# Kernel tuning notes

Measured on AMD Instinct MI355X. Metric: run time of the kernel, lower is better.

The kernel has to match this reference:

```python
import jax, jax.numpy as jnp
import numpy as np


def setup_inputs() -> dict:
    key = jax.random.key(0)
    ks = jax.random.split(key, 9)
    N, L, E, H = 8, 4096, 1024, 16
    D = E // H
    return {
        "values": jax.random.normal(ks[0], (N, L, E), dtype=jnp.float32),
        "keys": jax.random.normal(ks[1], (N, L, E), dtype=jnp.float32),
        "query": jax.random.normal(ks[2], (N, L, E), dtype=jnp.float32),
        "mask": jax.random.randint(ks[3], (1, 1, H, H), 0, 2, dtype=jnp.int32),
        "Wv": jax.random.normal(ks[4], (D, D), dtype=jnp.float32) / np.sqrt(D),
        "Wk": jax.random.normal(ks[5], (D, D), dtype=jnp.float32) / np.sqrt(D),
        "Wq": jax.random.normal(ks[6], (D, D), dtype=jnp.float32) / np.sqrt(D),
        "Wo": jax.random.normal(ks[7], (E, E), dtype=jnp.float32) / np.sqrt(E),
        "bo": jnp.zeros((E,), dtype=jnp.float32),
    }


def reference(values, keys, query, mask, Wv, Wk, Wq, Wo, bo):
    N, L, E = query.shape
    H = mask.shape[-1]          # heads
    D = E // H                  # head_dim
    # reshape to (N, L, H, D) then per-head Dense(head_dim) on last dim
    v = values.reshape(N, L, H, D) @ Wv
    k = keys.reshape(N, L, H, D) @ Wk
    q = query.reshape(N, L, H, D) @ Wq
    # Faithful to the source: keys transposed with perm [0,1,3,2], so matmul
    # batches over (N, L) and energy is a (H x H) matrix per position.
    energy = jnp.einsum("nlhd,nlgd->nlhg", q, k)  # (N, L, H, H)
    energy = jnp.where(mask == 0, jnp.float32(-1e20), energy)
    attention = jax.nn.softmax(energy / (E ** 0.5), axis=-1)
    out = jnp.einsum("nlhg,nlgd->nlhd", attention, v)  # (N, L, H, D)
    # source: transpose to (N, H, L, D) then reshape to (N, L, H*D)
    out = out.transpose(0, 2, 1, 3).reshape(N, L, H * D)
    out = out @ Wo + bo
    return out, attention
```

## Files before the change

kernel.cpp:

```cpp
#include <hip/hip_runtime.h>

typedef short short8 __attribute__((ext_vector_type(8)));
typedef float f32x4 __attribute__((ext_vector_type(4)));
typedef unsigned short u16;

#define MFMA16(a, b, c) __builtin_amdgcn_mfma_f32_16x16x32_bf16(a, b, c, 0, 0, 0)
#define GLD_LDS(g, l)                                                          \
  __builtin_amdgcn_global_load_lds(                                            \
      (__attribute__((address_space(1))) void*)(void*)(g),                     \
      (__attribute__((address_space(3))) void*)(l), 16, 0, 0)

__device__ __forceinline__ u16 f2bf(float f) {
  union { float f; unsigned u; } x; x.f = f;
  unsigned r = x.u + 0x7fffu + ((x.u >> 16) & 1u);
  return (u16)(r >> 16);
}

__device__ __forceinline__ short8 pack8(float4 a, float4 b) {
  short8 r;
  r[0] = (short)f2bf(a.x); r[1] = (short)f2bf(a.y);
  r[2] = (short)f2bf(a.z); r[3] = (short)f2bf(a.w);
  r[4] = (short)f2bf(b.x); r[5] = (short)f2bf(b.y);
  r[6] = (short)f2bf(b.z); r[7] = (short)f2bf(b.w);
  return r;
}

__global__ __launch_bounds__(256) void prep(const float* __restrict__ Wv,
                                            const float* __restrict__ Wk,
                                            const float* __restrict__ Wq,
                                            const float* __restrict__ Wo,
                                            u16* __restrict__ WoT2,
                                            u16* __restrict__ Mt) {
  __shared__ __align__(16) float A[64][65];
  __shared__ __align__(16) float B[64][68];
  const int t = threadIdx.x;
  const int r = t >> 2, c = (t & 3) * 16;
  if (blockIdx.x < 256) {
    const int tr = blockIdx.x >> 4, tc = blockIdx.x & 15;
#pragma unroll
    for (int u = 0; u < 4; ++u)
      *(float4*)&A[r][c + u * 4] = *(const float4*)(Wv + r * 64 + c + u * 4);
#pragma unroll
    for (int u = 0; u < 4; ++u)
      *(float4*)&B[r][c + u * 4] =
          *(const float4*)(Wo + (tr * 64 + r) * 1024 + tc * 64 + c + u * 4);
    __syncthreads();
    const int n = t & 63, i0 = (t >> 6) * 16;
    float acc[16];
#pragma unroll
    for (int ii = 0; ii < 16; ++ii) acc[ii] = 0.f;
    for (int j = 0; j < 64; ++j) {
      const float wo = B[j][n];
#pragma unroll
      for (int ii = 0; ii < 16; ++ii) acc[ii] += A[i0 + ii][j] * wo;
    }
    u16* dst = WoT2 + (size_t)(tc * 64 + n) * 1024 + tr * 64 + i0;
    short8 o0, o1;
#pragma unroll
    for (int jj = 0; jj < 8; ++jj) { o0[jj] = (short)f2bf(acc[jj]); o1[jj] = (short)f2bf(acc[8 + jj]); }
    *(short8*)(void*)dst = o0;
    *(short8*)(void*)(dst + 8) = o1;
  } else {
#pragma unroll
    for (int u = 0; u < 4; ++u)
      *(float4*)&A[r][c + u * 4] = *(const float4*)(Wq + r * 64 + c + u * 4);
#pragma unroll
    for (int u = 0; u < 4; ++u)
      *(float4*)&B[r][c + u * 4] = *(const float4*)(Wk + r * 64 + c + u * 4);
    __syncthreads();
    const int n = t & 63, k0 = (t >> 6) * 16;
    float acc[16];
#pragma unroll
    for (int ii = 0; ii < 16; ++ii) acc[ii] = 0.f;
    for (int d = 0; d < 64; ++d) {
      const float wk = B[n][d];
#pragma unroll
      for (int kk = 0; kk < 16; ++kk) acc[kk] += A[k0 + kk][d] * wk;
    }
    u16* dst = Mt + n * 64 + k0;
    short8 o0, o1;
#pragma unroll
    for (int jj = 0; jj < 8; ++jj) { o0[jj] = (short)f2bf(acc[jj]); o1[jj] = (short)f2bf(acc[8 + jj]); }
    *(short8*)(void*)dst = o0;
    *(short8*)(void*)(dst + 8) = o1;
  }
}

__global__ __launch_bounds__(256, 3) void attn_kernel(
    const float* __restrict__ values, const float* __restrict__ keys,
    const float* __restrict__ query, const int* __restrict__ mask,
    const u16* __restrict__ Mt, float* __restrict__ attn,
    u16* __restrict__ out2) {
  __shared__ __align__(16) u16 t_lds[4][16][72];
  __shared__ __align__(16) u16 vT_lds[4][64][24];
  __shared__ __align__(16) u16 p_lds[4][16][24];

  const int tid = threadIdx.x;
  const int w = tid >> 6, lane = tid & 63;
  const int g16 = lane & 15;
  const int q4 = lane >> 4;
  const int kbase = q4 * 8;
  const int mrow = q4 * 4;

  short8 mtf[2][4];
#pragma unroll
  for (int kb = 0; kb < 2; ++kb)
#pragma unroll
    for (int nc = 0; nc < 4; ++nc)
      mtf[kb][nc] =
          *(const short8*)(Mt + (nc * 16 + g16) * 64 + kb * 32 + kbase);

  bool mz[4];
#pragma unroll
  for (int r = 0; r < 4; ++r) mz[r] = (mask[(mrow + r) * 16 + g16] == 0);

  const f32x4 zero = {0.f, 0.f, 0.f, 0.f};
  const int gw = blockIdx.x * 4 + w;

#define LD4(dst, src, off)                                                     \
  {                                                                            \
    dst[0] = *(const float4*)((src) + (off));                                  \
    dst[1] = *(const float4*)((src) + (off) + 4);                              \
    dst[2] = *(const float4*)((src) + (off) + 32);                             \
    dst[3] = *(const float4*)((src) + (off) + 36);                             \
  }

  float4 qs[4], ks[4], vs[4];
  const int off0 = gw * 2 * 1024 + g16 * 64 + kbase;
  LD4(qs, query, off0);
  LD4(ks, keys, off0);
  LD4(vs, values, off0);

#pragma unroll 1
  for (int i = 0; i < 2; ++i) {
    const int p = gw * 2 + i;

    short8 aq0 = pack8(qs[0], qs[1]), aq1 = pack8(qs[2], qs[3]);
    short8 ak0 = pack8(ks[0], ks[1]), ak1 = pack8(ks[2], ks[3]);
    short8 av0 = pack8(vs[0], vs[1]), av1 = pack8(vs[2], vs[3]);
    if (i < 1) {
      const int off = off0 + 1024;
      LD4(qs, query, off);
      LD4(ks, keys, off);
      LD4(vs, values, off);
    }

    f32x4 tacc[4];
#pragma unroll
    for (int nc = 0; nc < 4; ++nc) {
      tacc[nc] = MFMA16(aq0, mtf[0][nc], zero);
      tacc[nc] = MFMA16(aq1, mtf[1][nc], tacc[nc]);
    }
#pragma unroll
    for (int nc = 0; nc < 4; ++nc)
#pragma unroll
      for (int r = 0; r < 4; ++r)
        t_lds[w][mrow + r][nc * 16 + g16] = f2bf(tacc[nc][r]);

#pragma unroll
    for (int j = 0; j < 8; ++j) {
      vT_lds[w][kbase + j][g16] = av0[j];
      vT_lds[w][32 + kbase + j][g16] = av1[j];
    }

    short8 ea0 = *(const short8*)&t_lds[w][g16][kbase];
    short8 ea1 = *(const short8*)&t_lds[w][g16][32 + kbase];
    f32x4 acce = MFMA16(ea0, ak0, zero);
    acce = MFMA16(ea1, ak1, acce);

    const float SC = 0.045084220027780106f;
    float av4[4];
#pragma unroll
    for (int r = 0; r < 4; ++r) {
      const float val = mz[r] ? -45.f : acce[r] * SC;
      const float pe = exp2f(val);
      float s = pe;
      s += __shfl_xor(s, 1, 16);
      s += __shfl_xor(s, 2, 16);
      s += __shfl_xor(s, 4, 16);
      s += __shfl_xor(s, 8, 16);
      av4[r] = pe * __builtin_amdgcn_rcpf(s);
    }

    float* ap = attn + (size_t)p * 256 + mrow * 16 + g16;
#pragma unroll
    for (int r = 0; r < 4; ++r) {
      ap[r * 16] = av4[r];
      p_lds[w][mrow + r][g16] = f2bf(av4[r]);
    }

    short8 pa;
    if (lane < 32) {
      pa = *(const short8*)&p_lds[w][g16][kbase];
    } else {
      short8 z = {0, 0, 0, 0, 0, 0, 0, 0};
      pa = z;
    }
    const int gsel = (lane < 32) ? kbase : 0;
#pragma unroll
    for (int nc = 0; nc < 4; ++nc) {
      short8 vb = *(const short8*)&vT_lds[w][nc * 16 + g16][gsel];
      f32x4 acco = MFMA16(pa, vb, zero);
#pragma unroll
      for (int r = 0; r < 4; ++r)
        t_lds[w][mrow + r][nc * 16 + g16] = f2bf(acco[r]);
    }

    const u16* orow = &t_lds[w][lane >> 2][(lane & 3) * 16];
    short8 s0 = *(const short8*)orow;
    short8 s1 = *(const short8*)(orow + 8);
    u16* dst = out2 + (size_t)p * 1024 + lane * 16;
    *(short8*)(void*)dst = s0;
    *(short8*)(void*)(dst + 8) = s1;
  }
#undef LD4
}

__global__ __launch_bounds__(256, 2) void gemm_kernel(
    const u16* __restrict__ A, const u16* __restrict__ BT,
    const float* __restrict__ bo, float* __restrict__ C) {
  __shared__ __align__(16) u16 As[128 * 32];
  __shared__ __align__(16) u16 Bs[128 * 32];
  const int t = threadIdx.x, lane = t & 63;
  const int g16 = lane & 15, q4 = lane >> 4;
  const int w = t >> 6, wm = w >> 1, wn = w & 1;
  const int bm = blockIdx.x & 255, bn = blockIdx.x >> 8;

  f32x4 acc[4][4];
  const f32x4 zero = {0.f, 0.f, 0.f, 0.f};
#pragma unroll
  for (int mt = 0; mt < 4; ++mt)
#pragma unroll
    for (int nt = 0; nt < 4; ++nt) acc[mt][nt] = zero;

  const int am = t >> 2, ak = (t & 3) * 8;
  const int R0 = bm * 128 + am;
  const int R1 = R0 + 64;
  const size_t base0 =
      ((size_t)((R0 >> 12) * 4096 + (R0 & 255) * 16)) * 1024 +
      ((R0 & 4095) >> 8) * 64;
  const size_t base1 =
      ((size_t)((R1 >> 12) * 4096 + (R1 & 255) * 16)) * 1024 +
      ((R1 & 4095) >> 8) * 64;
  const u16* ga0 = A + base0 + ak;
  const u16* ga1 = A + base1 + ak;
  const u16* gb = BT + (size_t)(bn * 128 + am) * 1024 + ak;
  u16* lA = &As[t * 8];
  u16* lB = &Bs[t * 8];

  for (int kt = 0; kt < 32; ++kt) {
    __syncthreads();
    const int aoff = (kt >> 1) * 1024 + (kt & 1) * 32;
    const int ko = kt * 32;
    GLD_LDS(ga0 + aoff, lA);
    GLD_LDS(ga1 + aoff, lA + 2048);
    GLD_LDS(gb + ko, lB);
    GLD_LDS(gb + 64 * 1024 + ko, lB + 2048);
    __syncthreads();

    short8 af[4], bf[4];
#pragma unroll
    for (int mt = 0; mt < 4; ++mt)
      af[mt] = *(const short8*)&As[(wm * 64 + mt * 16 + g16) * 32 + q4 * 8];
#pragma unroll
    for (int nt = 0; nt < 4; ++nt)
      bf[nt] = *(const short8*)&Bs[(wn * 64 + nt * 16 + g16) * 32 + q4 * 8];
#pragma unroll
    for (int mt = 0; mt < 4; ++mt)
#pragma unroll
      for (int nt = 0; nt < 4; ++nt)
        acc[mt][nt] = MFMA16(af[mt], bf[nt], acc[mt][nt]);
  }

#pragma unroll
  for (int nt = 0; nt < 4; ++nt) {
    const int col = bn * 128 + wn * 64 + nt * 16 + g16;
    const float bias = bo[col];
#pragma unroll
    for (int mt = 0; mt < 4; ++mt) {
#pragma unroll
      for (int r = 0; r < 4; ++r) {
        const int row = bm * 128 + wm * 64 + mt * 16 + q4 * 4 + r;
        C[(size_t)row * 1024 + col] = acc[mt][nt][r] + bias;
      }
    }
  }
}

extern "C" void kernel_launch(void* const* d_in, const int* in_sizes, int n_in,
                              void* d_out, int out_size, void* d_ws,
                              size_t ws_size, hipStream_t stream) {
  const float* values = (const float*)d_in[0];
  const float* keys   = (const float*)d_in[1];
  const float* query  = (const float*)d_in[2];
  const int*   mask   = (const int*)d_in[3];
  const float* Wv = (const float*)d_in[4];
  const float* Wk = (const float*)d_in[5];
  const float* Wq = (const float*)d_in[6];
  const float* Wo = (const float*)d_in[7];
  const float* bo = (const float*)d_in[8];

  float* out  = (float*)d_out;
  float* attn = out + 33554432;

  u16* out2 = (u16*)d_ws;
  u16* WoT2 = out2 + 33554432;
  u16* Mt   = WoT2 + 1048576;

  prep<<<257, 256, 0, stream>>>(Wv, Wk, Wq, Wo, WoT2, Mt);
  attn_kernel<<<4096, 256, 0, stream>>>(values, keys, query, mask, Mt, attn,
                                        out2);
  gemm_kernel<<<2048, 256, 0, stream>>>(out2, WoT2, bo, out);
}
```

Baseline: 231.8 us.

## Process one position per wave in attn kernel to raise occupancy

The attention kernel now handles one (n,l) position per wave instead of two. This removes the software-prefetch loop and the persistent Mt fragment registers, and it doubles the grid to 8192 blocks. The Mt fragments are loaded in two halves just before use to cut register pressure, the mask flags are packed into a bitfield, and launch bounds rise from 3 to 8 blocks per CU. The aim is more waves in flight to hide memory latency in this bandwidth-bound kernel. The cost is losing the explicit overlap of the next position's loads and reloading the Mt and mask data once per position.

```diff
diff --git a/kernel.cpp b/kernel.cpp
--- a/kernel.cpp
+++ b/kernel.cpp
@@ -86,7 +86,7 @@
   }
 }
 
-__global__ __launch_bounds__(256, 3) void attn_kernel(
+__global__ __launch_bounds__(256, 8) void attn_kernel(
     const float* __restrict__ values, const float* __restrict__ keys,
     const float* __restrict__ query, const int* __restrict__ mask,
     const u16* __restrict__ Mt, float* __restrict__ attn,
@@ -102,118 +102,116 @@
   const int kbase = q4 * 8;
   const int mrow = q4 * 4;
 
-  short8 mtf[2][4];
-#pragma unroll
-  for (int kb = 0; kb < 2; ++kb)
-#pragma unroll
-    for (int nc = 0; nc < 4; ++nc)
-      mtf[kb][nc] =
-          *(const short8*)(Mt + (nc * 16 + g16) * 64 + kb * 32 + kbase);
-
-  bool mz[4];
-#pragma unroll
-  for (int r = 0; r < 4; ++r) mz[r] = (mask[(mrow + r) * 16 + g16] == 0);
+  const int p = blockIdx.x * 4 + w;
+  const int off = p * 1024 + g16 * 64 + kbase;
+
+  int mzb = 0;
+#pragma unroll
+  for (int r = 0; r < 4; ++r)
+    mzb |= (mask[(mrow + r) * 16 + g16] == 0) ? (1 << r) : 0;
 
   const f32x4 zero = {0.f, 0.f, 0.f, 0.f};
-  const int gw = blockIdx.x * 4 + w;
-
-#define LD4(dst, src, off)                                                     \
-  {                                                                            \
-    dst[0] = *(const float4*)((src) + (off));                                  \
-    dst[1] = *(const float4*)((src) + (off) + 4);                              \
-    dst[2] = *(const float4*)((src) + (off) + 32);                             \
-    dst[3] = *(const float4*)((src) + (off) + 36);                             \
-  }
-
-  float4 qs[4], ks[4], vs[4];
-  const int off0 = gw * 2 * 1024 + g16 * 64 + kbase;
-  LD4(qs, query, off0);
-  LD4(ks, keys, off0);
-  LD4(vs, values, off0);
-
-#pragma unroll 1
-  for (int i = 0; i < 2; ++i) {
-    const int p = gw * 2 + i;
-
-    short8 aq0 = pack8(qs[0], qs[1]), aq1 = pack8(qs[2], qs[3]);
-    short8 ak0 = pack8(ks[0], ks[1]), ak1 = pack8(ks[2], ks[3]);
-    short8 av0 = pack8(vs[0], vs[1]), av1 = pack8(vs[2], vs[3]);
-    if (i < 1) {
-      const int off = off0 + 1024;
-      LD4(qs, query, off);
-      LD4(ks, keys, off);
-      LD4(vs, values, off);
-    }
-
-    f32x4 tacc[4];
-#pragma unroll
-    for (int nc = 0; nc < 4; ++nc) {
-      tacc[nc] = MFMA16(aq0, mtf[0][nc], zero);
-      tacc[nc] = MFMA16(aq1, mtf[1][nc], tacc[nc]);
-    }
-#pragma unroll
-    for (int nc = 0; nc < 4; ++nc)
-#pragma unroll
-      for (int r = 0; r < 4; ++r)
-        t_lds[w][mrow + r][nc * 16 + g16] = f2bf(tacc[nc][r]);
-
+
+  float4 qa0 = *(const float4*)(query + off);
+  float4 qa1 = *(const float4*)(query + off + 4);
+  float4 qb0 = *(const float4*)(query + off + 32);
+  float4 qb1 = *(const float4*)(query + off + 36);
+  float4 ka0 = *(const float4*)(keys + off);
+  float4 ka1 = *(const float4*)(keys + off + 4);
+  float4 kb0 = *(const float4*)(keys + off + 32);
+  float4 kb1 = *(const float4*)(keys + off + 36);
+  float4 va0 = *(const float4*)(values + off);
+  float4 va1 = *(const float4*)(values + off + 4);
+  float4 vb0 = *(const float4*)(values + off + 32);
+  float4 vb1 = *(const float4*)(values + off + 36);
+
+  short8 aq0 = pack8(qa0, qa1), aq1 = pack8(qb0, qb1);
+  short8 ak0 = pack8(ka0, ka1), ak1 = pack8(kb0, kb1);
+  {
+    short8 av0 = pack8(va0, va1), av1 = pack8(vb0, vb1);
 #pragma unroll
     for (int j = 0; j < 8; ++j) {
       vT_lds[w][kbase + j][g16] = av0[j];
       vT_lds[w][32 + kbase + j][g16] = av1[j];
     }
-
-    short8 ea0 = *(const short8*)&t_lds[w][g16][kbase];
-    short8 ea1 = *(const short8*)&t_lds[w][g16][32 + kbase];
-    f32x4 acce = MFMA16(ea0, ak0, zero);
-    acce = MFMA16(ea1, ak1, acce);
-
-    const float SC = 0.045084220027780106f;
-    float av4[4];
+  }
+
+  const u16* mtp = Mt + g16 * 64 + kbase;
+  {
+    short8 m00 = *(const short8*)(mtp + 0 * 1024);
+    short8 m01 = *(const short8*)(mtp + 0 * 1024 + 32);
+    short8 m10 = *(const short8*)(mtp + 1 * 1024);
+    short8 m11 = *(const short8*)(mtp + 1 * 1024 + 32);
+    f32x4 t0 = MFMA16(aq0, m00, zero);
+    t0 = MFMA16(aq1, m01, t0);
+    f32x4 t1 = MFMA16(aq0, m10, zero);
+    t1 = MFMA16(aq1, m11, t1);
 #pragma unroll
     for (int r = 0; r < 4; ++r) {
-      const float val = mz[r] ? -45.f : acce[r] * SC;
-      const float pe = exp2f(val);
-      float s = pe;
-      s += __shfl_xor(s, 1, 16);
-      s += __shfl_xor(s, 2, 16);
-      s += __shfl_xor(s, 4, 16);
-      s += __shfl_xor(s, 8, 16);
-      av4[r] = pe * __builtin_amdgcn_rcpf(s);
-    }
-
-    float* ap = attn + (size_t)p * 256 + mrow * 16 + g16;
+      t_lds[w][mrow + r][g16] = f2bf(t0[r]);
+      t_lds[w][mrow + r][16 + g16] = f2bf(t1[r]);
+    }
+  }
+  {
+    short8 m20 = *(const short8*)(mtp + 2 * 1024);
+    short8 m21 = *(const short8*)(mtp + 2 * 1024 + 32);
+    short8 m30 = *(const short8*)(mtp + 3 * 1024);
+    short8 m31 = *(const short8*)(mtp + 3 * 1024 + 32);
+    f32x4 t2 = MFMA16(aq0, m20, zero);
+    t2 = MFMA16(aq1, m21, t2);
+    f32x4 t3 = MFMA16(aq0, m30, zero);
+    t3 = MFMA16(aq1, m31, t3);
 #pragma unroll
     for (int r = 0; r < 4; ++r) {
-      ap[r * 16] = av4[r];
-      p_lds[w][mrow + r][g16] = f2bf(av4[r]);
-    }
-
-    short8 pa;
-    if (lane < 32) {
-      pa = *(const short8*)&p_lds[w][g16][kbase];
-    } else {
-      short8 z = {0, 0, 0, 0, 0, 0, 0, 0};
-      pa = z;
-    }
-    const int gsel = (lane < 32) ? kbase : 0;
-#pragma unroll
-    for (int nc = 0; nc < 4; ++nc) {
-      short8 vb = *(const short8*)&vT_lds[w][nc * 16 + g16][gsel];
-      f32x4 acco = MFMA16(pa, vb, zero);
-#pragma unroll
-      for (int r = 0; r < 4; ++r)
-        t_lds[w][mrow + r][nc * 16 + g16] = f2bf(acco[r]);
-    }
-
-    const u16* orow = &t_lds[w][lane >> 2][(lane & 3) * 16];
-    short8 s0 = *(const short8*)orow;
-    short8 s1 = *(const short8*)(orow + 8);
-    u16* dst = out2 + (size_t)p * 1024 + lane * 16;
-    *(short8*)(void*)dst = s0;
-    *(short8*)(void*)(dst + 8) = s1;
-  }
-#undef LD4
+      t_lds[w][mrow + r][32 + g16] = f2bf(t2[r]);
+      t_lds[w][mrow + r][48 + g16] = f2bf(t3[r]);
+    }
+  }
+
+  short8 ea0 = *(const short8*)&t_lds[w][g16][kbase];
+  short8 ea1 = *(const short8*)&t_lds[w][g16][32 + kbase];
+  f32x4 acce = MFMA16(ea0, ak0, zero);
+  acce = MFMA16(ea1, ak1, acce);
+
+  const float SC = 0.045084220027780106f;
+  float* ap = attn + (size_t)p * 256 + mrow * 16 + g16;
+#pragma unroll
+  for (int r = 0; r < 4; ++r) {
+    const float val = ((mzb >> r) & 1) ? -45.f : acce[r] * SC;
+    const float pe = exp2f(val);
+    float s = pe;
+    s += __shfl_xor(s, 1, 16);
+    s += __shfl_xor(s, 2, 16);
+    s += __shfl_xor(s, 4, 16);
+    s += __shfl_xor(s, 8, 16);
+    const float a = pe * __builtin_amdgcn_rcpf(s);
+    ap[r * 16] = a;
+    p_lds[w][mrow + r][g16] = f2bf(a);
+  }
+
+  short8 pa;
+  if (lane < 32) {
+    pa = *(const short8*)&p_lds[w][g16][kbase];
+  } else {
+    short8 z = {0, 0, 0, 0, 0, 0, 0, 0};
+    pa = z;
+  }
+  const int gsel = (lane < 32) ? kbase : 0;
+#pragma unroll
+  for (int nc = 0; nc < 4; ++nc) {
+    short8 vb = *(const short8*)&vT_lds[w][nc * 16 + g16][gsel];
+    f32x4 acco = MFMA16(pa, vb, zero);
+#pragma unroll
+    for (int r = 0; r < 4; ++r)
+      t_lds[w][mrow + r][nc * 16 + g16] = f2bf(acco[r]);
+  }
+
+  const u16* orow = &t_lds[w][lane >> 2][(lane & 3) * 16];
+  short8 s0 = *(const short8*)orow;
+  short8 s1 = *(const short8*)(orow + 8);
+  u16* dst = out2 + (size_t)p * 1024 + lane * 16;
+  *(short8*)(void*)dst = s0;
+  *(short8*)(void*)(dst + 8) = s1;
 }
 
 __global__ __launch_bounds__(256, 2) void gemm_kernel(
@@ -308,7 +306,7 @@
   u16* Mt   = WoT2 + 1048576;
 
   prep<<<257, 256, 0, stream>>>(Wv, Wk, Wq, Wo, WoT2, Mt);
-  attn_kernel<<<4096, 256, 0, stream>>>(values, keys, query, mask, Mt, attn,
+  attn_kernel<<<8192, 256, 0, stream>>>(values, keys, query, mask, Mt, attn,
                                         out2);
   gemm_kernel<<<2048, 256, 0, stream>>>(out2, WoT2, bo, out);
 }
```

Result: no change. 229.1 us (-1.2%).

## Coalesce attention-kernel loads via LDS staging and process one position per wave

Applied to the files above, without the earlier changes.

Each wave now handles one (n,l) position instead of two, and the grid doubles. Q/K/V rows are read with fully coalesced float4 loads and staged through LDS as bf16 before the MFMA fragment reads. The Mt matrix and the mask are loaded once per block into LDS. Attention probabilities are also staged so each lane writes one contiguous float4. The changes target uncoalesced global access and redundant per-wave Mt reads, at the cost of more LDS traffic, a block-wide barrier, and losing the software prefetch of the second position.

```diff
diff --git a/kernel.cpp b/kernel.cpp
--- a/kernel.cpp
+++ b/kernel.cpp
@@ -1,6 +1,7 @@
 #include <hip/hip_runtime.h>
 
 typedef short short8 __attribute__((ext_vector_type(8)));
+typedef short short4v __attribute__((ext_vector_type(4)));
 typedef float f32x4 __attribute__((ext_vector_type(4)));
 typedef unsigned short u16;
 
@@ -16,12 +17,10 @@
   return (u16)(r >> 16);
 }
 
-__device__ __forceinline__ short8 pack8(float4 a, float4 b) {
-  short8 r;
-  r[0] = (short)f2bf(a.x); r[1] = (short)f2bf(a.y);
-  r[2] = (short)f2bf(a.z); r[3] = (short)f2bf(a.w);
-  r[4] = (short)f2bf(b.x); r[5] = (short)f2bf(b.y);
-  r[6] = (short)f2bf(b.z); r[7] = (short)f2bf(b.w);
+__device__ __forceinline__ short4v pack4(f32x4 a) {
+  short4v r;
+  r[0] = (short)f2bf(a[0]); r[1] = (short)f2bf(a[1]);
+  r[2] = (short)f2bf(a[2]); r[3] = (short)f2bf(a[3]);
   return r;
 }
 
@@ -86,14 +85,16 @@
   }
 }
 
-__global__ __launch_bounds__(256, 3) void attn_kernel(
+__global__ __launch_bounds__(256, 4) void attn_kernel(
     const float* __restrict__ values, const float* __restrict__ keys,
     const float* __restrict__ query, const int* __restrict__ mask,
     const u16* __restrict__ Mt, float* __restrict__ attn,
     u16* __restrict__ out2) {
-  __shared__ __align__(16) u16 t_lds[4][16][72];
-  __shared__ __align__(16) u16 vT_lds[4][64][24];
-  __shared__ __align__(16) u16 p_lds[4][16][24];
+  __shared__ __align__(16) u16 x1[4][16][68];
+  __shared__ __align__(16) u16 x2[4][16][68];
+  __shared__ __align__(16) u16 vT[4][64][24];
+  __shared__ __align__(16) u16 mt_lds[64][68];
+  __shared__ int mask_lds[256];
 
   const int tid = threadIdx.x;
   const int w = tid >> 6, lane = tid & 63;
@@ -102,118 +103,123 @@
   const int kbase = q4 * 8;
   const int mrow = q4 * 4;
 
+  {
+    const short8* mg = (const short8*)Mt;
+    short8 a0 = mg[tid];
+    short8 a1 = mg[256 + tid];
+    *(short8*)&mt_lds[tid >> 3][(tid & 7) * 8] = a0;
+    const int g1 = 256 + tid;
+    *(short8*)&mt_lds[g1 >> 3][(g1 & 7) * 8] = a1;
+    mask_lds[tid] = mask[tid];
+  }
+  __syncthreads();
+
+  int mzb = 0;
+#pragma unroll
+  for (int r = 0; r < 4; ++r)
+    mzb |= (mask_lds[(mrow + r) * 16 + g16] == 0) ? (1 << r) : 0;
+
+  const f32x4 zero = {0.f, 0.f, 0.f, 0.f};
+  const int p = blockIdx.x * 4 + w;
+
+  const f32x4* qv = (const f32x4*)(query + (size_t)p * 1024);
+  const f32x4* kv = (const f32x4*)(keys + (size_t)p * 1024);
+  const f32x4* vv = (const f32x4*)(values + (size_t)p * 1024);
+  f32x4 qf0 = qv[lane], qf1 = qv[64 + lane], qf2 = qv[128 + lane], qf3 = qv[192 + lane];
+  f32x4 kf0 = kv[lane], kf1 = kv[64 + lane], kf2 = kv[128 + lane], kf3 = kv[192 + lane];
+  f32x4 vf0 = vv[lane], vf1 = vv[64 + lane], vf2 = vv[128 + lane], vf3 = vv[192 + lane];
+
+  const int wr = lane >> 4;
+  const int wc = (lane & 15) * 4;
+  *(short4v*)&x1[w][0 + wr][wc] = pack4(qf0);
+  *(short4v*)&x1[w][4 + wr][wc] = pack4(qf1);
+  *(short4v*)&x1[w][8 + wr][wc] = pack4(qf2);
+  *(short4v*)&x1[w][12 + wr][wc] = pack4(qf3);
+  *(short4v*)&x2[w][0 + wr][wc] = pack4(kf0);
+  *(short4v*)&x2[w][4 + wr][wc] = pack4(kf1);
+  *(short4v*)&x2[w][8 + wr][wc] = pack4(kf2);
+  *(short4v*)&x2[w][12 + wr][wc] = pack4(kf3);
+#pragma unroll
+  for (int i = 0; i < 4; ++i) {
+    vT[w][wc + i][0 + wr] = f2bf(vf0[i]);
+    vT[w][wc + i][4 + wr] = f2bf(vf1[i]);
+    vT[w][wc + i][8 + wr] = f2bf(vf2[i]);
+    vT[w][wc + i][12 + wr] = f2bf(vf3[i]);
+  }
+
+  short8 aq0 = *(const short8*)&x1[w][g16][kbase];
+  short8 aq1 = *(const short8*)&x1[w][g16][32 + kbase];
+  short8 ak0 = *(const short8*)&x2[w][g16][kbase];
+  short8 ak1 = *(const short8*)&x2[w][g16][32 + kbase];
   short8 mtf[2][4];
 #pragma unroll
   for (int kb = 0; kb < 2; ++kb)
 #pragma unroll
     for (int nc = 0; nc < 4; ++nc)
-      mtf[kb][nc] =
-          *(const short8*)(Mt + (nc * 16 + g16) * 64 + kb * 32 + kbase);
-
-  bool mz[4];
-#pragma unroll
-  for (int r = 0; r < 4; ++r) mz[r] = (mask[(mrow + r) * 16 + g16] == 0);
-
-  const f32x4 zero = {0.f, 0.f, 0.f, 0.f};
-  const int gw = blockIdx.x * 4 + w;
-
-#define LD4(dst, src, off)                                                     \
-  {                                                                            \
-    dst[0] = *(const float4*)((src) + (off));                                  \
-    dst[1] = *(const float4*)((src) + (off) + 4);                              \
-    dst[2] = *(const float4*)((src) + (off) + 32);                             \
-    dst[3] = *(const float4*)((src) + (off) + 36);                             \
-  }
-
-  float4 qs[4], ks[4], vs[4];
-  const int off0 = gw * 2 * 1024 + g16 * 64 + kbase;
-  LD4(qs, query, off0);
-  LD4(ks, keys, off0);
-  LD4(vs, values, off0);
-
-#pragma unroll 1
-  for (int i = 0; i < 2; ++i) {
-    const int p = gw * 2 + i;
-
-    short8 aq0 = pack8(qs[0], qs[1]), aq1 = pack8(qs[2], qs[3]);
-    short8 ak0 = pack8(ks[0], ks[1]), ak1 = pack8(ks[2], ks[3]);
-    short8 av0 = pack8(vs[0], vs[1]), av1 = pack8(vs[2], vs[3]);
-    if (i < 1) {
-      const int off = off0 + 1024;
-      LD4(qs, query, off);
-      LD4(ks, keys, off);
-      LD4(vs, values, off);
-    }
-
-    f32x4 tacc[4];
-#pragma unroll
-    for (int nc = 0; nc < 4; ++nc) {
-      tacc[nc] = MFMA16(aq0, mtf[0][nc], zero);
-      tacc[nc] = MFMA16(aq1, mtf[1][nc], tacc[nc]);
-    }
-#pragma unroll
-    for (int nc = 0; nc < 4; ++nc)
-#pragma unroll
-      for (int r = 0; r < 4; ++r)
-        t_lds[w][mrow + r][nc * 16 + g16] = f2bf(tacc[nc][r]);
-
-#pragma unroll
-    for (int j = 0; j < 8; ++j) {
-      vT_lds[w][kbase + j][g16] = av0[j];
-      vT_lds[w][32 + kbase + j][g16] = av1[j];
-    }
-
-    short8 ea0 = *(const short8*)&t_lds[w][g16][kbase];
-    short8 ea1 = *(const short8*)&t_lds[w][g16][32 + kbase];
-    f32x4 acce = MFMA16(ea0, ak0, zero);
-    acce = MFMA16(ea1, ak1, acce);
-
-    const float SC = 0.045084220027780106f;
-    float av4[4];
-#pragma unroll
-    for (int r = 0; r < 4; ++r) {
-      const float val = mz[r] ? -45.f : acce[r] * SC;
-      const float pe = exp2f(val);
-      float s = pe;
-      s += __shfl_xor(s, 1, 16);
-      s += __shfl_xor(s, 2, 16);
-      s += __shfl_xor(s, 4, 16);
-      s += __shfl_xor(s, 8, 16);
-      av4[r] = pe * __builtin_amdgcn_rcpf(s);
-    }
-
-    float* ap = attn + (size_t)p * 256 + mrow * 16 + g16;
-#pragma unroll
-    for (int r = 0; r < 4; ++r) {
-      ap[r * 16] = av4[r];
-      p_lds[w][mrow + r][g16] = f2bf(av4[r]);
-    }
-
-    short8 pa;
-    if (lane < 32) {
-      pa = *(const short8*)&p_lds[w][g16][kbase];
-    } else {
-      short8 z = {0, 0, 0, 0, 0, 0, 0, 0};
-      pa = z;
-    }
-    const int gsel = (lane < 32) ? kbase : 0;
-#pragma unroll
-    for (int nc = 0; nc < 4; ++nc) {
-      short8 vb = *(const short8*)&vT_lds[w][nc * 16 + g16][gsel];
-      f32x4 acco = MFMA16(pa, vb, zero);
-#pragma unroll
-      for (int r = 0; r < 4; ++r)
-        t_lds[w][mrow + r][nc * 16 + g16] = f2bf(acco[r]);
-    }
-
-    const u16* orow = &t_lds[w][lane >> 2][(lane & 3) * 16];
-    short8 s0 = *(const short8*)orow;
-    short8 s1 = *(const short8*)(orow + 8);
-    u16* dst = out2 + (size_t)p * 1024 + lane * 16;
+      mtf[kb][nc] = *(const short8*)&mt_lds[nc * 16 + g16][kb * 32 + kbase];
+
+  f32x4 tacc[4];
+#pragma unroll
+  for (int nc = 0; nc < 4; ++nc) {
+    tacc[nc] = MFMA16(aq0, mtf[0][nc], zero);
+    tacc[nc] = MFMA16(aq1, mtf[1][nc], tacc[nc]);
+  }
+#pragma unroll
+  for (int nc = 0; nc < 4; ++nc)
+#pragma unroll
+    for (int r = 0; r < 4; ++r)
+      x1[w][mrow + r][nc * 16 + g16] = f2bf(tacc[nc][r]);
+
+  short8 ea0 = *(const short8*)&x1[w][g16][kbase];
+  short8 ea1 = *(const short8*)&x1[w][g16][32 + kbase];
+  f32x4 acce = MFMA16(ea0, ak0, zero);
+  acce = MFMA16(ea1, ak1, acce);
+
+  const float SC = 0.045084220027780106f;
+  float* x1f = (float*)&x1[w][0][0];
+#pragma unroll
+  for (int r = 0; r < 4; ++r) {
+    const float val = ((mzb >> r) & 1) ? -45.f : acce[r] * SC;
+    const float pe = exp2f(val);
+    float s = pe;
+    s += __shfl_xor(s, 1, 16);
+    s += __shfl_xor(s, 2, 16);
+    s += __shfl_xor(s, 4, 16);
+    s += __shfl_xor(s, 8, 16);
+    const float a = pe * __builtin_amdgcn_rcpf(s);
+    x1f[(mrow + r) * 34 + g16] = a;
+    x2[w][mrow + r][g16] = f2bf(a);
+  }
+
+  {
+    f32x4 av = *(const f32x4*)&x1f[(lane >> 2) * 34 + (lane & 3) * 4];
+    *(f32x4*)(attn + (size_t)p * 256 + lane * 4) = av;
+  }
+
+  short8 pa;
+  if (lane < 32) {
+    pa = *(const short8*)&x2[w][g16][kbase];
+  } else {
+    short8 z = {0, 0, 0, 0, 0, 0, 0, 0};
+    pa = z;
+  }
+  const int gsel = (lane < 32) ? kbase : 0;
+#pragma unroll
+  for (int nc = 0; nc < 4; ++nc) {
+    short8 vb = *(const short8*)&vT[w][nc * 16 + g16][gsel];
+    f32x4 acco = MFMA16(pa, vb, zero);
+#pragma unroll
+    for (int r = 0; r < 4; ++r)
+      x1[w][mrow + r][nc * 16 + g16] = f2bf(acco[r]);
+  }
+
+  {
+    short8 s0 = *(const short8*)&x1[w][lane >> 3][(lane & 7) * 8];
+    short8 s1 = *(const short8*)&x1[w][8 + (lane >> 3)][(lane & 7) * 8];
+    u16* dst = out2 + (size_t)p * 1024 + lane * 8;
     *(short8*)(void*)dst = s0;
-    *(short8*)(void*)(dst + 8) = s1;
-  }
-#undef LD4
+    *(short8*)(void*)(dst + 512) = s1;
+  }
 }
 
 __global__ __launch_bounds__(256, 2) void gemm_kernel(
@@ -308,7 +314,7 @@
   u16* Mt   = WoT2 + 1048576;
 
   prep<<<257, 256, 0, stream>>>(Wv, Wk, Wq, Wo, WoT2, Mt);
-  attn_kernel<<<4096, 256, 0, stream>>>(values, keys, query, mask, Mt, attn,
+  attn_kernel<<<8192, 256, 0, stream>>>(values, keys, query, mask, Mt, attn,
                                         out2);
   gemm_kernel<<<2048, 256, 0, stream>>>(out2, WoT2, bo, out);
 }
```

After: 233.7 us. No clear change (+0.8%).
